# Kernel tuning notes

Measured on AMD Instinct MI355X. Metric: run time of the kernel, lower is better.

## Reference

```python
import jax, jax.numpy as jnp
import numpy as np

EPS = 1e-5
QMAX = 127.0

def setup_inputs() -> dict:
    key = jax.random.key(0)
    k_x, k_w = jax.random.split(key)
    B, S, DIN, DOUT = 8, 2048, 4096, 4096
    x = jax.random.normal(k_x, (B, S, DIN), dtype=jnp.float32)
    # Learned full-precision weight (kaiming-normal, fan_out) then ternarized,
    # mimicking BitLinear._post_init -> terniarize(params).
    std = np.sqrt(2.0 / DOUT)
    w_fp = jax.random.normal(k_w, (DOUT, DIN), dtype=jnp.float32) * std
    scale_w = 1.0 / jnp.clip(jnp.mean(jnp.abs(w_fp)), 1e-5)   # scalar, matches terniarize
    w_ternary = jnp.clip(jnp.round(w_fp * scale_w), -1.0, 1.0)  # values in {-1,0,1}, stored as f32
    gamma = jnp.ones((DIN,), dtype=jnp.float32)                 # RMSNorm weight
    bias = jnp.zeros((DOUT,), dtype=jnp.float32)                # init.constant_(bias, 0)
    return {"x": x, "w_ternary": w_ternary, "scale_w": scale_w, "gamma": gamma, "bias": bias}

def reference(x, w_ternary, scale_w, gamma, bias):
    # 1) RMSNorm over last dim (in_features)
    var = jnp.mean(jnp.square(x), axis=-1, keepdims=True)
    xn = x * jax.lax.rsqrt(var + EPS) * gamma
    # 2) bitmat: per-token absmax int8 quantization of activations
    scale_x = QMAX / jnp.clip(jnp.max(jnp.abs(xn), axis=-1, keepdims=True), 1e-5)  # [B,S,1]
    xq = jnp.clip(jnp.round(xn * scale_x), -128.0, 127.0)
    # 3) ternary matmul (int math expressed in f32) + inline dequant by scale_x*scale_w
    acc = jnp.einsum('bsk,ok->bso', xq, w_ternary)  # [B,S,DOUT]
    out = acc / (scale_x * scale_w)
    # 4) bias
    return out + bias
```

## Files before the change

### kernel.cpp

```cpp
#include <hip/hip_runtime.h>
#include <cstdint>

#define DIN 4096
#define DOUT 4096
#define QMAXF 127.0f

typedef int v4i __attribute__((ext_vector_type(4)));
typedef unsigned int u32;

__device__ __forceinline__ void async16(const void* g, void* l) {
  __builtin_amdgcn_global_load_lds((const __attribute__((address_space(1))) u32*)g,
                                   (__attribute__((address_space(3))) u32*)l,
                                   16, 0, 0);
}

__device__ __forceinline__ int clamp_q(float v) {
  int i = (int)rintf(v);
  return i < -128 ? -128 : (i > 127 ? 127 : i);
}

__global__ __launch_bounds__(256) void wconvert_kernel(const float* __restrict__ w,
                                                       int8_t* __restrict__ wq) {
  int t = blockIdx.x * 256 + threadIdx.x;
  float4 v = ((const float4*)w)[t];
  int b0 = ((int)v.x) & 255, b1 = ((int)v.y) & 255;
  int b2 = ((int)v.z) & 255, b3 = ((int)v.w) & 255;
  ((int*)wq)[t] = b0 | (b1 << 8) | (b2 << 16) | (b3 << 24);
}

__global__ __launch_bounds__(256) void rmsnorm_quant_kernel(
    const float* __restrict__ x, const float* __restrict__ gamma,
    const float* __restrict__ scale_w_ptr, int8_t* __restrict__ xq,
    float* __restrict__ inv_scale) {
  const int token = blockIdx.x;
  const float* xr = x + (size_t)token * DIN;
  const int t = threadIdx.x;

  float4 xv[4], gv[4];
  float ss = 0.f, amax = 0.f;
#pragma unroll
  for (int i = 0; i < 4; ++i) {
    const int idx = (i * 256 + t) * 4;
    xv[i] = *(const float4*)(xr + idx);
    gv[i] = *(const float4*)(gamma + idx);
    ss += xv[i].x * xv[i].x + xv[i].y * xv[i].y + xv[i].z * xv[i].z + xv[i].w * xv[i].w;
    amax = fmaxf(amax, fabsf(xv[i].x * gv[i].x));
    amax = fmaxf(amax, fabsf(xv[i].y * gv[i].y));
    amax = fmaxf(amax, fabsf(xv[i].z * gv[i].z));
    amax = fmaxf(amax, fabsf(xv[i].w * gv[i].w));
  }
#pragma unroll
  for (int o = 32; o > 0; o >>= 1) {
    ss += __shfl_down(ss, o);
    amax = fmaxf(amax, __shfl_down(amax, o));
  }
  __shared__ float s_ss[4], s_am[4];
  const int wave = t >> 6, lane = t & 63;
  if (lane == 0) { s_ss[wave] = ss; s_am[wave] = amax; }
  __syncthreads();
  const float tot = s_ss[0] + s_ss[1] + s_ss[2] + s_ss[3];
  const float mx = fmaxf(fmaxf(s_am[0], s_am[1]), fmaxf(s_am[2], s_am[3]));
  const float rstd = rsqrtf(tot * (1.0f / DIN) + 1e-5f);
  const float absmax = fmaxf(mx * rstd, 1e-5f);
  const float qscale = rstd * (QMAXF / absmax);
  if (t == 0) inv_scale[token] = absmax / (QMAXF * scale_w_ptr[0]);

  int* qr = (int*)(xq + (size_t)token * DIN);
#pragma unroll
  for (int i = 0; i < 4; ++i) {
    const int idx4 = i * 256 + t;
    int b0 = clamp_q(xv[i].x * gv[i].x * qscale) & 255;
    int b1 = clamp_q(xv[i].y * gv[i].y * qscale) & 255;
    int b2 = clamp_q(xv[i].z * gv[i].z * qscale) & 255;
    int b3 = clamp_q(xv[i].w * gv[i].w * qscale) & 255;
    qr[idx4] = b0 | (b1 << 8) | (b2 << 16) | (b3 << 24);
  }
}

#define BM 128
#define BN 128
#define BK 128

__global__ __launch_bounds__(256) void gemm_i8_kernel(
    const int8_t* __restrict__ xq, const int8_t* __restrict__ wq,
    const float* __restrict__ inv_scale, const float* __restrict__ bias,
    float* __restrict__ out) {
  __shared__ int8_t As[BM * BK];
  __shared__ int8_t Bs[BN * BK];

  const int t = threadIdx.x;
  const int wave = t >> 6;
  const int lane = t & 63;
  const int m0 = blockIdx.y * BM;
  const int n0 = blockIdx.x * BN;

  int srow[4], scol[4];
#pragma unroll
  for (int i = 0; i < 4; ++i) {
    const int p = i * 256 + t;
    srow[i] = p >> 3;
    scol[i] = ((p - (p >> 3)) & 7) * 16;
  }

  const int8_t* Ag = xq + (size_t)m0 * DIN;
  const int8_t* Bg = wq + (size_t)n0 * DIN;

  v4i acc[4][4];
#pragma unroll
  for (int mi = 0; mi < 4; ++mi)
#pragma unroll
    for (int ni = 0; ni < 4; ++ni) acc[mi][ni] = (v4i){0, 0, 0, 0};

  const int wm = (wave >> 1) * 64;
  const int wn = (wave & 1) * 64;
  const int fr = lane & 15;
  const int q = lane >> 4;

  int offA[2][4], offB[2][4];
#pragma unroll
  for (int s = 0; s < 2; ++s)
#pragma unroll
    for (int j = 0; j < 4; ++j) {
      const int sw = ((s * 4 + q + fr) & 7) * 16;
      offA[s][j] = (wm + j * 16 + fr) * BK + sw;
      offB[s][j] = (wn + j * 16 + fr) * BK + sw;
    }

  for (int k0 = 0; k0 < DIN; k0 += BK) {
    __syncthreads();
#pragma unroll
    for (int i = 0; i < 4; ++i)
      async16(Ag + (size_t)srow[i] * DIN + k0 + scol[i], &As[i * 4096 + t * 16]);
#pragma unroll
    for (int i = 0; i < 4; ++i)
      async16(Bg + (size_t)srow[i] * DIN + k0 + scol[i], &Bs[i * 4096 + t * 16]);
    __syncthreads();

#pragma unroll
    for (int s = 0; s < 2; ++s) {
      v4i a[4], b[4];
#pragma unroll
      for (int j = 0; j < 4; ++j) a[j] = *(const v4i*)(&As[offA[s][j]]);
#pragma unroll
      for (int j = 0; j < 4; ++j) b[j] = *(const v4i*)(&Bs[offB[s][j]]);
#pragma unroll
      for (int mi = 0; mi < 4; ++mi)
#pragma unroll
        for (int ni = 0; ni < 4; ++ni)
          acc[mi][ni] = __builtin_amdgcn_mfma_i32_16x16x64_i8(a[mi], b[ni], acc[mi][ni], 0, 0, 0);
    }
  }

  const int col = lane & 15;
  const int rb = (lane >> 4) * 4;
#pragma unroll
  for (int mi = 0; mi < 4; ++mi) {
    float sc[4];
#pragma unroll
    for (int r = 0; r < 4; ++r) sc[r] = inv_scale[m0 + wm + mi * 16 + rb + r];
#pragma unroll
    for (int ni = 0; ni < 4; ++ni) {
      const int gc = n0 + wn + ni * 16 + col;
      const float bb = bias[gc];
#pragma unroll
      for (int r = 0; r < 4; ++r) {
        const int gr = m0 + wm + mi * 16 + rb + r;
        out[(size_t)gr * DOUT + gc] = (float)acc[mi][ni][r] * sc[r] + bb;
      }
    }
  }
}

extern "C" void kernel_launch(void* const* d_in, const int* in_sizes, int n_in,
                              void* d_out, int out_size, void* d_ws, size_t ws_size,
                              hipStream_t stream) {
  const float* x       = (const float*)d_in[0];
  const float* w       = (const float*)d_in[1];
  const float* scale_w = (const float*)d_in[2];
  const float* gamma   = (const float*)d_in[3];
  const float* bias    = (const float*)d_in[4];
  float* out = (float*)d_out;
  const int M = in_sizes[0] / DIN;

  int8_t* wq = (int8_t*)d_ws;
  int8_t* xq = wq + (size_t)DOUT * DIN;
  float* inv_scale = (float*)(xq + (size_t)M * DIN);

  hipLaunchKernelGGL(wconvert_kernel, dim3((DOUT * DIN) / (256 * 4)), dim3(256), 0, stream,
                     w, wq);
  hipLaunchKernelGGL(rmsnorm_quant_kernel, dim3(M), dim3(256), 0, stream,
                     x, gamma, scale_w, xq, inv_scale);
  hipLaunchKernelGGL(gemm_i8_kernel, dim3(DOUT / BN, M / BM), dim3(256), 0, stream,
                     xq, wq, inv_scale, bias, out);
}
```

Baseline: 831.0 us.

## Rewrite int8 GEMM with 256x256 tiles and 4-stage async LDS pipeline

Replaces the 128x128 single-buffered GEMM with a 256x256 tile handled by 512 threads (8 waves, each covering a 128x64 sub-tile). A 4-deep ring of LDS buffers is prefetched with global_load_lds, and explicit vmcnt waits let loads overlap the MFMA work. The body is interleaved with barriers and s_setprio to schedule MFMA against staging. The larger tile raises data reuse but uses 128KB of LDS and many accumulator registers, which risks lower occupancy.

```diff
diff --git a/kernel.cpp b/kernel.cpp
--- a/kernel.cpp
+++ b/kernel.cpp
@@ -77,94 +77,124 @@
   }
 }
 
-#define BM 128
-#define BN 128
-#define BK 128
-
-__global__ __launch_bounds__(256) void gemm_i8_kernel(
+#define BT 256
+#define BK 64
+
+__global__ __launch_bounds__(512, 2) void gemm_i8_kernel(
     const int8_t* __restrict__ xq, const int8_t* __restrict__ wq,
     const float* __restrict__ inv_scale, const float* __restrict__ bias,
     float* __restrict__ out) {
-  __shared__ int8_t As[BM * BK];
-  __shared__ int8_t Bs[BN * BK];
+  __shared__ __align__(16) int8_t As[4][BT * BK];
+  __shared__ __align__(16) int8_t Bs[4][BT * BK];
 
   const int t = threadIdx.x;
-  const int wave = t >> 6;
-  const int lane = t & 63;
-  const int m0 = blockIdx.y * BM;
-  const int n0 = blockIdx.x * BN;
-
-  int srow[4], scol[4];
-#pragma unroll
-  for (int i = 0; i < 4; ++i) {
-    const int p = i * 256 + t;
-    srow[i] = p >> 3;
-    scol[i] = ((p - (p >> 3)) & 7) * 16;
+  const int wave = t >> 6, lane = t & 63;
+  const int m0 = blockIdx.y * BT, n0 = blockIdx.x * BT;
+  const int wm = wave >> 2;
+  const int wn = wave & 3;
+  const int fr = lane & 15, q = lane >> 4;
+
+  int srow[2], scol[2];
+#pragma unroll
+  for (int i = 0; i < 2; ++i) {
+    const int p = i * 512 + t;
+    srow[i] = p >> 2;
+    scol[i] = (((p & 3) - (srow[i] >> 1)) & 3) * 16;
   }
 
   const int8_t* Ag = xq + (size_t)m0 * DIN;
   const int8_t* Bg = wq + (size_t)n0 * DIN;
 
-  v4i acc[4][4];
-#pragma unroll
-  for (int mi = 0; mi < 4; ++mi)
+  const int swz = ((q + (fr >> 1)) & 3) * 16;
+  int offA[8], offB[4];
+#pragma unroll
+  for (int mi = 0; mi < 8; ++mi) offA[mi] = (wm * 128 + mi * 16 + fr) * BK + swz;
+#pragma unroll
+  for (int ni = 0; ni < 4; ++ni) offB[ni] = (wn * 64 + ni * 16 + fr) * BK + swz;
+
+  v4i acc[8][4];
+#pragma unroll
+  for (int mi = 0; mi < 8; ++mi)
 #pragma unroll
     for (int ni = 0; ni < 4; ++ni) acc[mi][ni] = (v4i){0, 0, 0, 0};
 
-  const int wm = (wave >> 1) * 64;
-  const int wn = (wave & 1) * 64;
-  const int fr = lane & 15;
-  const int q = lane >> 4;
-
-  int offA[2][4], offB[2][4];
-#pragma unroll
-  for (int s = 0; s < 2; ++s)
-#pragma unroll
-    for (int j = 0; j < 4; ++j) {
-      const int sw = ((s * 4 + q + fr) & 7) * 16;
-      offA[s][j] = (wm + j * 16 + fr) * BK + sw;
-      offB[s][j] = (wn + j * 16 + fr) * BK + sw;
-    }
-
-  for (int k0 = 0; k0 < DIN; k0 += BK) {
-    __syncthreads();
-#pragma unroll
-    for (int i = 0; i < 4; ++i)
-      async16(Ag + (size_t)srow[i] * DIN + k0 + scol[i], &As[i * 4096 + t * 16]);
-#pragma unroll
-    for (int i = 0; i < 4; ++i)
-      async16(Bg + (size_t)srow[i] * DIN + k0 + scol[i], &Bs[i * 4096 + t * 16]);
-    __syncthreads();
-
-#pragma unroll
-    for (int s = 0; s < 2; ++s) {
-      v4i a[4], b[4];
-#pragma unroll
-      for (int j = 0; j < 4; ++j) a[j] = *(const v4i*)(&As[offA[s][j]]);
-#pragma unroll
-      for (int j = 0; j < 4; ++j) b[j] = *(const v4i*)(&Bs[offB[s][j]]);
-#pragma unroll
-      for (int mi = 0; mi < 4; ++mi)
-#pragma unroll
-        for (int ni = 0; ni < 4; ++ni)
-          acc[mi][ni] = __builtin_amdgcn_mfma_i32_16x16x64_i8(a[mi], b[ni], acc[mi][ni], 0, 0, 0);
-    }
-  }
+#define STAGE_A(buf, kt)                                                        \
+  do {                                                                          \
+    async16(Ag + (size_t)srow[0] * DIN + (kt) * BK + scol[0], &As[buf][t * 16]);\
+    async16(Ag + (size_t)srow[1] * DIN + (kt) * BK + scol[1],                   \
+            &As[buf][8192 + t * 16]);                                           \
+  } while (0)
+#define STAGE_B(buf, kt)                                                        \
+  do {                                                                          \
+    async16(Bg + (size_t)srow[0] * DIN + (kt) * BK + scol[0], &Bs[buf][t * 16]);\
+    async16(Bg + (size_t)srow[1] * DIN + (kt) * BK + scol[1],                   \
+            &Bs[buf][8192 + t * 16]);                                           \
+  } while (0)
+
+#define VMCNT8 asm volatile("s_waitcnt vmcnt(8)" ::: "memory")
+#define VMCNT4 asm volatile("s_waitcnt vmcnt(4)" ::: "memory")
+#define VMCNT0 asm volatile("s_waitcnt vmcnt(0)" ::: "memory")
+
+#define KTILE(bufidx, DO_STAGE, kt, WAITSTMT)                                   \
+  do {                                                                          \
+    const int8_t* Ab = &As[bufidx][0];                                          \
+    const int8_t* Bb = &Bs[bufidx][0];                                          \
+    v4i a[4], b[4];                                                             \
+    _Pragma("unroll") for (int j = 0; j < 4; ++j)                               \
+        b[j] = *(const v4i*)(Bb + offB[j]);                                     \
+    _Pragma("unroll") for (int j = 0; j < 4; ++j)                               \
+        a[j] = *(const v4i*)(Ab + offA[j]);                                     \
+    if (DO_STAGE) STAGE_A(((kt) + 3) & 3, (kt) + 3);                            \
+    __builtin_amdgcn_s_barrier();                                               \
+    __builtin_amdgcn_s_setprio(1);                                              \
+    _Pragma("unroll") for (int mi = 0; mi < 4; ++mi)                            \
+        _Pragma("unroll") for (int ni = 0; ni < 4; ++ni)                        \
+            acc[mi][ni] = __builtin_amdgcn_mfma_i32_16x16x64_i8(                \
+                a[mi], b[ni], acc[mi][ni], 0, 0, 0);                            \
+    __builtin_amdgcn_s_setprio(0);                                              \
+    __builtin_amdgcn_s_barrier();                                               \
+    _Pragma("unroll") for (int j = 0; j < 4; ++j)                               \
+        a[j] = *(const v4i*)(Ab + offA[4 + j]);                                 \
+    if (DO_STAGE) STAGE_B(((kt) + 3) & 3, (kt) + 3);                            \
+    __builtin_amdgcn_s_barrier();                                               \
+    __builtin_amdgcn_s_setprio(1);                                              \
+    _Pragma("unroll") for (int mi = 0; mi < 4; ++mi)                            \
+        _Pragma("unroll") for (int ni = 0; ni < 4; ++ni)                        \
+            acc[4 + mi][ni] = __builtin_amdgcn_mfma_i32_16x16x64_i8(            \
+                a[mi], b[ni], acc[4 + mi][ni], 0, 0, 0);                        \
+    __builtin_amdgcn_s_setprio(0);                                              \
+    WAITSTMT;                                                                   \
+    __builtin_amdgcn_s_barrier();                                               \
+  } while (0)
+
+  STAGE_A(0, 0); STAGE_B(0, 0);
+  STAGE_A(1, 1); STAGE_B(1, 1);
+  STAGE_A(2, 2); STAGE_B(2, 2);
+  VMCNT8;
+  __builtin_amdgcn_s_barrier();
+
+  const int NT = DIN / BK;
+#pragma unroll 1
+  for (int kt = 0; kt < NT - 3; ++kt)
+    KTILE(kt & 3, true, kt, VMCNT8);
+  KTILE(1, false, 0, VMCNT4);
+  KTILE(2, false, 0, VMCNT0);
+  KTILE(3, false, 0, (void)0);
 
   const int col = lane & 15;
   const int rb = (lane >> 4) * 4;
 #pragma unroll
-  for (int mi = 0; mi < 4; ++mi) {
+  for (int mi = 0; mi < 8; ++mi) {
     float sc[4];
 #pragma unroll
-    for (int r = 0; r < 4; ++r) sc[r] = inv_scale[m0 + wm + mi * 16 + rb + r];
+    for (int r = 0; r < 4; ++r) sc[r] = inv_scale[m0 + wm * 128 + mi * 16 + rb + r];
 #pragma unroll
     for (int ni = 0; ni < 4; ++ni) {
-      const int gc = n0 + wn + ni * 16 + col;
+      const int gc = n0 + wn * 64 + ni * 16 + col;
       const float bb = bias[gc];
 #pragma unroll
       for (int r = 0; r < 4; ++r) {
-        const int gr = m0 + wm + mi * 16 + rb + r;
+        const int gr = m0 + wm * 128 + mi * 16 + rb + r;
         out[(size_t)gr * DOUT + gc] = (float)acc[mi][ni][r] * sc[r] + bb;
       }
     }
@@ -190,6 +220,6 @@
                      w, wq);
   hipLaunchKernelGGL(rmsnorm_quant_kernel, dim3(M), dim3(256), 0, stream,
                      x, gamma, scale_w, xq, inv_scale);
-  hipLaunchKernelGGL(gemm_i8_kernel, dim3(DOUT / BN, M / BM), dim3(256), 0, stream,
+  hipLaunchKernelGGL(gemm_i8_kernel, dim3(DOUT / BT, M / BT), dim3(512), 0, stream,
                      xq, wq, inv_scale, bias, out);
 }
```

After: 788.6 us. -5.1%, faster.
